# Performance work log

Measured on AMD Instinct MI355X. Metric: run time of the kernel, lower is better.

Reference implementation:

```python
import jax, jax.numpy as jnp
from jax import lax
import numpy as np

B, IN, J, S, F, O, C, KS = 8, 8, 8, 187, 64, 64, 67, 15


def _ln(x, eps=1e-5):
    m = jnp.mean(x, axis=-1, keepdims=True)
    v = jnp.mean((x - m) ** 2, axis=-1, keepdims=True)
    return (x - m) / jnp.sqrt(v + eps)


def setup_inputs() -> dict:
    key = jax.random.key(0)
    ks = jax.random.split(key, 8)
    x_in = jax.random.normal(ks[0], (B, IN, S, F), jnp.float32)
    proj_x_prev = jax.random.normal(ks[1], (B, IN, S, O), jnp.float32)
    lin = jnp.linspace(-1.0, 1.0, C, dtype=jnp.float32)
    spline_weights = jnp.broadcast_to(lin, (IN, J, C)) + 0.01 * jax.random.normal(ks[2], (IN, J, C), jnp.float32)
    tau = 0.1 * jax.random.normal(ks[3], (IN, J), jnp.float32) + 0.1
    temperature = jnp.asarray(1.0, jnp.float32)
    omiga = jnp.full((IN, J), 0.2, jnp.float32)
    W2 = jax.random.normal(ks[4], (J, F, O), jnp.float32) * (1.0 / np.sqrt(F))
    b_param = 0.02 * jax.random.normal(ks[5], (J, S, O), jnp.float32)
    ln_scale = jnp.ones((J, F), jnp.float32)
    ln_bias = jnp.zeros((J, F), jnp.float32)
    alpha = jnp.ones((J,), jnp.float32)
    beta = jnp.ones((J,), jnp.float32)
    theta = jnp.ones((J,), jnp.float32)
    gamma = jnp.ones((J,), jnp.float32)
    w3 = 0.1 * jax.random.normal(ks[6], (J, O, KS), jnp.float32)  # depthwise conv kernels
    return dict(x_in=x_in, proj_x_prev=proj_x_prev, spline_weights=spline_weights, tau=tau,
                temperature=temperature, omiga=omiga, W2=W2, b_param=b_param, ln_scale=ln_scale,
                ln_bias=ln_bias, alpha=alpha, beta=beta, theta=theta, gamma=gamma, w3=w3)


def reference(x_in, proj_x_prev, spline_weights, tau, temperature, omiga, W2, b_param,
              ln_scale, ln_bias, alpha, beta, theta, gamma, w3):
    b, in_n, seq, feat = x_in.shape
    out_n, nC = spline_weights.shape[1], spline_weights.shape[2]
    kk = w3.shape[-1]
    # --- cubic B-spline basis ---
    h = 2.0 / (nC - 1)
    grid = jnp.linspace(-1.0, 1.0, nC, dtype=x_in.dtype)
    max_val = jnp.max(jnp.abs(x_in)) + 1e-8
    xn = jnp.clip(x_in / max_val * 0.95, -0.99, 0.99)
    dist = jnp.abs(xn[..., None] - grid) / h  # [b,in,seq,feat,C]
    basis = jax.nn.relu(2.0 - dist) ** 3 / 6.0 - jax.nn.relu(1.0 - dist) ** 3 * (4.0 / 6.0)
    spline_mapping = jnp.einsum('bisfc,ijc->bijsf', basis, spline_weights)
    activated = spline_mapping + jnp.abs(omiga)[None, :, :, None, None] * x_in[:, :, None]
    # --- energy-threshold gating ---
    energies = jnp.mean(activated ** 2, axis=(-1, -2))  # [b,in,out]
    tau_a = jnp.abs(tau)[None]
    t_val = jnp.abs(temperature) * np.sqrt(seq / 256.0) + 1e-4
    sqrtE = jnp.sqrt(energies + 1e-8)
    mask = jax.nn.sigmoid((sqrtE - tau_a) / t_val)  # [b,in,out]
    mult = sqrtE / (tau_a + 1e-8)
    wp = proj_x_prev[:, :, None] * (mult * mask)[..., None, None]  # [b,in,out,seq,d]
    d = wp.shape[-1]
    mid = in_n // 2
    Kt = wp[:, 0::2].transpose(0, 2, 3, 1, 4).reshape(b, out_n, seq, mid * d)
    Qt = wp[:, 1::2].transpose(0, 2, 3, 1, 4).reshape(b, out_n, seq, mid * d)
    Kt, Qt = _ln(Kt), _ln(Qt)
    raw = jnp.einsum('bjse,bjte->bjst', Kt, Qt)
    W1 = jax.nn.softmax(raw / (np.sqrt(mid * d) * t_val), axis=-1)  # [b,out,seq,seq]
    combined = jnp.einsum('bijsf,bij->bjsf', activated, mask)  # [b,out,seq,feat]
    # --- SplineWeightLayer (vectorized over out_n) ---
    xln = _ln(combined) * ln_scale[None, :, None, :] + ln_bias[None, :, None, :]
    x_prime = jnp.einsum('bjsh,jho->bjso', xln, W2) + b_param[None]  # [b,out,seq,O]
    o = x_prime.shape[-1]
    xt = x_prime.transpose(0, 2, 1, 3).reshape(b, seq, out_n * o)
    ker = w3.transpose(2, 0, 1).reshape(kk, 1, out_n * o)
    w3f = lax.conv_general_dilated(xt, ker, (1,), [(kk // 2, kk // 2)],
                                   dimension_numbers=('NWC', 'WIO', 'NWC'),
                                   feature_group_count=out_n * o)
    w3f = w3f.reshape(b, seq, out_n, o).transpose(0, 2, 1, 3)
    eye = jnp.eye(seq, dtype=x_in.dtype)
    attn_kernel = jnp.abs(beta)[None, :, None, None] * W1 + jnp.abs(alpha)[None, :, None, None] * eye
    global_part = jnp.einsum('bjst,bjto->bjso', attn_kernel, x_prime)
    spatial = global_part + jnp.abs(theta)[None, :, None, None] * w3f
    out = spatial + gamma[None, :, None, None] * combined  # residual_proj is Identity (F==O)
    return out, x_prime
```

## Files before the change

kernel.cpp:

```cpp
#include <hip/hip_runtime.h>
#include <math.h>

#define B_N 8
#define IN_N 8
#define J_N 8
#define S_N 187
#define F_N 64
#define O_N 64
#define C_N 67
#define KS_N 15
#define SF_N (S_N * F_N)
#define E_N 256
#define ROWS_N (B_N * J_N * S_N)
#define SQRT_SF 0.85467470f

#define NT_SPL 47
#define NCOMB 376
#define NKTQT 2992
#define NRAW 576
#define NXPR 768
#define NMAXP 256

typedef __attribute__((ext_vector_type(8))) _Float16 half8;
typedef __attribute__((ext_vector_type(4))) _Float16 half4;
typedef __attribute__((ext_vector_type(4))) float floatx4;

__device__ __forceinline__ float wave_sum(float v) {
#pragma unroll
  for (int off = 32; off > 0; off >>= 1) v += __shfl_down(v, off, 64);
  return __shfl(v, 0, 64);
}
__device__ __forceinline__ float wave_max(float v) {
#pragma unroll
  for (int off = 32; off > 0; off >>= 1) v = fmaxf(v, __shfl_down(v, off, 64));
  return __shfl(v, 0, 64);
}
__device__ __forceinline__ float lane_bc(float v, int l) {
  return __int_as_float(__builtin_amdgcn_readlane(__float_as_int(v), l));
}
__device__ __forceinline__ float bspline(float d) {
  float t2 = fmaxf(2.f - d, 0.f);
  float t1 = fmaxf(1.f - d, 0.f);
  return t2 * t2 * t2 * (1.f / 6.f) - t1 * t1 * t1 * (4.f / 6.f);
}
__device__ __forceinline__ float get_inv095(const float* __restrict__ maxp) {
  int lane = threadIdx.x & 63;
  float m = 0.f;
#pragma unroll
  for (int k = 0; k < NMAXP / 64; k++) m = fmaxf(m, maxp[lane + k * 64]);
  return 0.95f / (wave_max(m) + 1e-8f);
}

__global__ void k_maxabs(const float4* __restrict__ x, float* __restrict__ maxp, int n4) {
  __shared__ float red[4];
  int tid = blockIdx.x * 256 + threadIdx.x;
  float m = 0.f;
  for (int i = tid; i < n4; i += gridDim.x * 256) {
    float4 v = x[i];
    m = fmaxf(m, fmaxf(fmaxf(fabsf(v.x), fabsf(v.y)), fmaxf(fabsf(v.z), fabsf(v.w))));
  }
  m = wave_max(m);
  if ((threadIdx.x & 63) == 0) red[threadIdx.x >> 6] = m;
  __syncthreads();
  if (threadIdx.x == 0)
    maxp[blockIdx.x] = fmaxf(fmaxf(red[0], red[1]), fmaxf(red[2], red[3]));
}

__global__ void k_spline(const float* __restrict__ x_in, const float* __restrict__ sw,
                         const float* __restrict__ omiga, const float* __restrict__ maxp,
                         float* __restrict__ act, float* __restrict__ esum_p) {
  int tile = blockIdx.x, bi = blockIdx.y;
  int i = bi & 7;
  __shared__ float wl[J_N * C_N];
  __shared__ float aom[J_N];
  __shared__ float red[4 * J_N];
  for (int t = threadIdx.x; t < J_N * C_N; t += 256) wl[t] = sw[i * J_N * C_N + t];
  if (threadIdx.x < J_N) aom[threadIdx.x] = fabsf(omiga[i * J_N + threadIdx.x]);
  int lane = threadIdx.x & 63, wid = threadIdx.x >> 6;
  float inv = get_inv095(maxp);
  __syncthreads();
  int idx = tile * 256 + threadIdx.x;
  float e[J_N] = {0, 0, 0, 0, 0, 0, 0, 0};
  if (idx < SF_N) {
    float x = x_in[(long)bi * SF_N + idx];
    float xn = fminf(fmaxf(x * inv, -0.99f), 0.99f);
    float u = (xn + 1.f) * 33.f;
    int c0 = (int)floorf(u) - 1;
    float sm[J_N] = {0, 0, 0, 0, 0, 0, 0, 0};
#pragma unroll
    for (int kk = 0; kk < 4; kk++) {
      int c = c0 + kk;
      if (c >= 0 && c < C_N) {
        float bas = bspline(fabsf(u - (float)c));
#pragma unroll
        for (int j = 0; j < J_N; j++) sm[j] += bas * wl[j * C_N + c];
      }
    }
#pragma unroll
    for (int j = 0; j < J_N; j++) {
      float a = sm[j] + aom[j] * x;
      act[((long)(bi * 8 + j)) * SF_N + idx] = a;
      e[j] = a * a;
    }
  }
#pragma unroll
  for (int j = 0; j < J_N; j++) {
    float v = e[j];
#pragma unroll
    for (int off = 32; off > 0; off >>= 1) v += __shfl_down(v, off, 64);
    if (lane == 0) red[wid * J_N + j] = v;
  }
  __syncthreads();
  if (threadIdx.x < J_N)
    esum_p[(long)(bi * 8 + threadIdx.x) * 48 + tile] =
        red[threadIdx.x] + red[8 + threadIdx.x] + red[16 + threadIdx.x] + red[24 + threadIdx.x];
}

__global__ void k_reduceE(const float* __restrict__ esum_p, const float* __restrict__ tau,
                          const float* __restrict__ temp, float* __restrict__ g_mask,
                          float* __restrict__ g_g) {
  int t = blockIdx.x * 256 + threadIdx.x;
  if (t >= 512) return;
  int i = (t >> 3) & 7, j = t & 7;
  const float* p = esum_p + (long)t * 48;
  float s = 0.f;
#pragma unroll
  for (int k = 0; k < NT_SPL; k++) s += p[k];
  float E = s * (1.f / (float)SF_N);
  float sE = sqrtf(E + 1e-8f);
  float ta = fabsf(tau[i * 8 + j]);
  float tv = fabsf(temp[0]) * SQRT_SF + 1e-4f;
  float mask = 1.f / (1.f + expf(-(sE - ta) / tv));
  g_mask[t] = mask;
  g_g[t] = (sE / (ta + 1e-8f)) * mask;
}

__global__ void k_mid2(const float* __restrict__ act, const float* __restrict__ g_mask,
                       const float* __restrict__ g_g, const float* __restrict__ proj,
                       float* __restrict__ comb,
                       _Float16* __restrict__ khi, _Float16* __restrict__ klo,
                       _Float16* __restrict__ qhi, _Float16* __restrict__ qlo) {
  __shared__ float mk[64];
  int lane = threadIdx.x & 63;
  if (blockIdx.x < NCOMB) {
    int b = blockIdx.x / 47, tile = blockIdx.x - b * 47;
    if (threadIdx.x < 64) mk[threadIdx.x] = g_mask[b * 64 + threadIdx.x];
    __syncthreads();
    int idx = tile * 256 + threadIdx.x;
    if (idx < SF_N) {
      float cb[J_N] = {0, 0, 0, 0, 0, 0, 0, 0};
#pragma unroll
      for (int i = 0; i < IN_N; i++) {
#pragma unroll
        for (int j = 0; j < J_N; j++)
          cb[j] += mk[i * 8 + j] * act[((long)((b * 8 + i) * 8 + j)) * SF_N + idx];
      }
#pragma unroll
      for (int j = 0; j < J_N; j++) comb[(b * J_N + j) * SF_N + idx] = cb[j];
    }
  } else {
    int w = threadIdx.x >> 6;
    int gr = (blockIdx.x - NCOMB) * 4 + w;
    int bj = gr / S_N, s = gr - bj * S_N;
    int b = bj >> 3, j = bj & 7;
    int ig = lane >> 4;
    int f4 = (lane & 15) * 4;
    int iK = b * 8 + 2 * ig;
    int iQ = iK + 1;
    float gK = g_g[iK * 8 + j];
    float gQ = g_g[iQ * 8 + j];
    float4 kr = *(const float4*)(proj + ((long)iK * S_N + s) * 64 + f4);
    float4 qr = *(const float4*)(proj + ((long)iQ * S_N + s) * 64 + f4);
    float kv[4] = {kr.x * gK, kr.y * gK, kr.z * gK, kr.w * gK};
    float qv[4] = {qr.x * gQ, qr.y * gQ, qr.z * gQ, qr.w * gQ};
    float mkv = wave_sum(kv[0] + kv[1] + kv[2] + kv[3]) * (1.f / 256.f);
    float mqv = wave_sum(qv[0] + qv[1] + qv[2] + qv[3]) * (1.f / 256.f);
    float vk = 0.f, vq = 0.f;
#pragma unroll
    for (int q = 0; q < 4; q++) {
      float dk = kv[q] - mkv; vk += dk * dk;
      float dq = qv[q] - mqv; vq += dq * dq;
    }
    vk = wave_sum(vk) * (1.f / 256.f);
    vq = wave_sum(vq) * (1.f / 256.f);
    float ik = 1.f / sqrtf(vk + 1e-5f);
    float iq = 1.f / sqrtf(vq + 1e-5f);
    long base = (long)gr * E_N + lane * 4;
    half4 hk4, lk4, hq4, lq4;
#pragma unroll
    for (int q = 0; q < 4; q++) {
      float fk = (kv[q] - mkv) * ik;
      float fq = (qv[q] - mqv) * iq;
      _Float16 hk = (_Float16)fk;
      _Float16 hq = (_Float16)fq;
      hk4[q] = hk; lk4[q] = (_Float16)(fk - (float)hk);
      hq4[q] = hq; lq4[q] = (_Float16)(fq - (float)hq);
    }
    *(half4*)(khi + base) = hk4;
    *(half4*)(klo + base) = lk4;
    *(half4*)(qhi + base) = hq4;
    *(half4*)(qlo + base) = lq4;
  }
}

__global__ void k_gemm(const _Float16* __restrict__ khi, const _Float16* __restrict__ klo,
                       const _Float16* __restrict__ qhi, const _Float16* __restrict__ qlo,
                       const float* __restrict__ temp, float* __restrict__ w1,
                       const float* __restrict__ comb, const float* __restrict__ W2,
                       const float* __restrict__ bparam, const float* __restrict__ lns,
                       const float* __restrict__ lnb, float* __restrict__ xprime) {
  __shared__ float smem[64 * 64 + 128];
  int lane = threadIdx.x & 63;
  if (blockIdx.x < NRAW) {
    int idx = blockIdx.x;
    int st = idx % 3, tt = (idx / 3) % 3, bj = idx / 9;
    int wave = threadIdx.x >> 6;
    int quad = lane >> 4, m16 = lane & 15;
    int ebase = quad * 8;
    int mrow = st * 64 + wave * 16 + m16;
    if (mrow > S_N - 1) mrow = S_N - 1;
    long aoff = ((long)bj * S_N + mrow) * E_N + ebase;
    const _Float16* ah_p = khi + aoff;
    const _Float16* al_p = klo + aoff;
    const _Float16* bh_p[4];
    const _Float16* bl_p[4];
#pragma unroll
    for (int n = 0; n < 4; n++) {
      int t = tt * 64 + n * 16 + m16;
      if (t > S_N - 1) t = S_N - 1;
      long boff = ((long)bj * S_N + t) * E_N + ebase;
      bh_p[n] = qhi + boff;
      bl_p[n] = qlo + boff;
    }
    floatx4 acc[4] = {};
    for (int ec = 0; ec < 8; ec++) {
      half8 ah = *(const half8*)(ah_p + ec * 32);
      half8 al = *(const half8*)(al_p + ec * 32);
#pragma unroll
      for (int n = 0; n < 4; n++) {
        half8 bh = *(const half8*)(bh_p[n] + ec * 32);
        half8 bl = *(const half8*)(bl_p[n] + ec * 32);
        acc[n] = __builtin_amdgcn_mfma_f32_16x16x32_f16(ah, bh, acc[n], 0, 0, 0);
        acc[n] = __builtin_amdgcn_mfma_f32_16x16x32_f16(al, bh, acc[n], 0, 0, 0);
        acc[n] = __builtin_amdgcn_mfma_f32_16x16x32_f16(ah, bl, acc[n], 0, 0, 0);
      }
    }
    float tv = fabsf(temp[0]) * SQRT_SF + 1e-4f;
    float scale = 1.f / (16.f * tv);
#pragma unroll
    for (int n = 0; n < 4; n++) {
      int t = tt * 64 + n * 16 + m16;
      if (t >= S_N) continue;
#pragma unroll
      for (int r = 0; r < 4; r++) {
        int s = st * 64 + wave * 16 + quad * 4 + r;
        if (s < S_N) w1[((long)bj * S_N + s) * S_N + t] = acc[n][r] * scale;
      }
    }
  } else {
    int q = blockIdx.x - NRAW;
    int tile = q % 12, bj = q / 12;
    int j = bj & 7;
    float* w2s = smem;
    float* lss = smem + 4096;
    float* lbs = smem + 4160;
    const float4* wg = (const float4*)(W2 + j * 4096);
    float4* ws4 = (float4*)w2s;
    for (int idx = threadIdx.x; idx < 1024; idx += 256) ws4[idx] = wg[idx];
    if (threadIdx.x < 64) {
      lss[threadIdx.x] = lns[j * 64 + threadIdx.x];
      lbs[threadIdx.x] = lnb[j * 64 + threadIdx.x];
    }
    __syncthreads();
    int w = threadIdx.x >> 6;
    int sbase = tile * 16 + w * 4;
    float xln[4], acc[4];
#pragma unroll
    for (int rr = 0; rr < 4; rr++) {
      int s = sbase + rr;
      int sc = (s < S_N) ? s : S_N - 1;
      float x = comb[((long)bj * S_N + sc) * 64 + lane];
      float m = wave_sum(x) * (1.f / 64.f);
      float d = x - m;
      float var = wave_sum(d * d) * (1.f / 64.f);
      xln[rr] = d / sqrtf(var + 1e-5f) * lss[lane] + lbs[lane];
      acc[rr] = bparam[(j * S_N + sc) * 64 + lane];
    }
#pragma unroll
    for (int h = 0; h < 64; h++) {
      float w2v = w2s[h * 64 + lane];
#pragma unroll
      for (int rr = 0; rr < 4; rr++) acc[rr] += lane_bc(xln[rr], h) * w2v;
    }
#pragma unroll
    for (int rr = 0; rr < 4; rr++) {
      int s = sbase + rr;
      if (s < S_N) xprime[((long)bj * S_N + s) * 64 + lane] = acc[rr];
    }
  }
}

__global__ void k_final(const float* __restrict__ xprime, const float* __restrict__ w1,
                        const float* __restrict__ comb, const float* __restrict__ w3,
                        const float* __restrict__ alpha, const float* __restrict__ beta,
                        const float* __restrict__ theta, const float* __restrict__ gamma,
                        float* __restrict__ out) {
  int tile = blockIdx.x, bj = blockIdx.y;
  int j = bj & 7;
  __shared__ float w1t[16 * 188];
  int s0 = tile * 16;
  for (int idx = threadIdx.x; idx < 16 * S_N; idx += 256) {
    int r = idx / S_N, t = idx - r * S_N;
    int srow = s0 + r;
    w1t[r * 188 + t] = (srow < S_N) ? w1[((long)bj * S_N + srow) * S_N + t] : 0.f;
  }
  __syncthreads();
  int w = threadIdx.x >> 6, o = threadIdx.x & 63;
#pragma unroll
  for (int rr = 0; rr < 4; rr++) {
    float* row = &w1t[(w * 4 + rr) * 188];
    float v[3];
    float m = -1e30f;
#pragma unroll
    for (int q = 0; q < 3; q++) {
      int t = o + q * 64;
      v[q] = (t < S_N) ? row[t] : -1e30f;
      m = fmaxf(m, v[q]);
    }
    m = wave_max(m);
    float ssum = 0.f;
#pragma unroll
    for (int q = 0; q < 3; q++) {
      int t = o + q * 64;
      float e = (t < S_N) ? expf(v[q] - m) : 0.f;
      v[q] = e;
      ssum += e;
    }
    ssum = wave_sum(ssum);
    float invs = 1.f / ssum;
#pragma unroll
    for (int q = 0; q < 3; q++) {
      int t = o + q * 64;
      if (t < S_N) row[t] = v[q] * invs;
    }
  }
  float w3c[KS_N];
#pragma unroll
  for (int k = 0; k < KS_N; k++) w3c[k] = w3[j * 64 * KS_N + o * KS_N + k];
  const float* xpg = xprime + (long)bj * (S_N * 64);
  float aa = fabsf(alpha[j]), ba = fabsf(beta[j]), ta = fabsf(theta[j]), gv = gamma[j];
  float acc[4] = {0.f, 0.f, 0.f, 0.f};
  for (int t = 0; t < 184; t += 4) {
    float x0 = xpg[t * 64 + o];
    float x1 = xpg[(t + 1) * 64 + o];
    float x2 = xpg[(t + 2) * 64 + o];
    float x3 = xpg[(t + 3) * 64 + o];
#pragma unroll
    for (int rr = 0; rr < 4; rr++) {
      float4 wv = *(const float4*)&w1t[(w * 4 + rr) * 188 + t];
      acc[rr] += wv.x * x0 + wv.y * x1 + wv.z * x2 + wv.w * x3;
    }
  }
#pragma unroll
  for (int t = 184; t < S_N; t++) {
    float xv = xpg[t * 64 + o];
#pragma unroll
    for (int rr = 0; rr < 4; rr++) acc[rr] += w1t[(w * 4 + rr) * 188 + t] * xv;
  }
#pragma unroll
  for (int rr = 0; rr < 4; rr++) {
    int s = s0 + w * 4 + rr;
    if (s >= S_N) continue;
    float conv = 0.f;
#pragma unroll
    for (int k = 0; k < KS_N; k++) {
      int si = s + k - 7;
      if (si >= 0 && si < S_N) conv += xpg[si * 64 + o] * w3c[k];
    }
    float res = ba * acc[rr] + aa * xpg[s * 64 + o] + ta * conv +
                gv * comb[((long)bj * S_N + s) * 64 + o];
    out[((long)bj * S_N + s) * 64 + o] = res;
  }
}

extern "C" void kernel_launch(void* const* d_in, const int* in_sizes, int n_in,
                              void* d_out, int out_size, void* d_ws, size_t ws_size,
                              hipStream_t stream) {
  const float* x_in   = (const float*)d_in[0];
  const float* proj   = (const float*)d_in[1];
  const float* sw     = (const float*)d_in[2];
  const float* tau    = (const float*)d_in[3];
  const float* temp   = (const float*)d_in[4];
  const float* omiga  = (const float*)d_in[5];
  const float* W2     = (const float*)d_in[6];
  const float* bparam = (const float*)d_in[7];
  const float* lns    = (const float*)d_in[8];
  const float* lnb    = (const float*)d_in[9];
  const float* alpha  = (const float*)d_in[10];
  const float* beta   = (const float*)d_in[11];
  const float* theta  = (const float*)d_in[12];
  const float* gamma  = (const float*)d_in[13];
  const float* w3     = (const float*)d_in[14];

  float* out = (float*)d_out;
  float* xprime = out + B_N * J_N * S_N * O_N;

  float* wsf = (float*)d_ws;
  float* maxp   = wsf;
  float* esum_p = wsf + 512;
  float* g_mask = wsf + 512 + 512 * 48;
  float* g_g    = g_mask + 512;
  float* act    = g_g + 512;
  const long RE = (long)ROWS_N * E_N;
  _Float16* khi = (_Float16*)(act + (long)64 * 8 * SF_N);
  _Float16* klo = khi + RE;
  _Float16* qhi = klo + RE;
  _Float16* qlo = qhi + RE;
  float* w1   = (float*)khi + 2 * RE;
  float* comb = w1 + (long)B_N * J_N * S_N * S_N;

  k_maxabs<<<NMAXP, 256, 0, stream>>>((const float4*)x_in, maxp, (B_N * IN_N * S_N * F_N) / 4);
  k_spline<<<dim3(NT_SPL, 64), 256, 0, stream>>>(x_in, sw, omiga, maxp, act, esum_p);
  k_reduceE<<<2, 256, 0, stream>>>(esum_p, tau, temp, g_mask, g_g);
  k_mid2<<<NCOMB + NKTQT, 256, 0, stream>>>(act, g_mask, g_g, proj, comb,
                                            khi, klo, qhi, qlo);
  k_gemm<<<NRAW + NXPR, 256, 0, stream>>>(khi, klo, qhi, qlo, temp, w1,
                                          comb, W2, bparam, lns, lnb, xprime);
  k_final<<<dim3(12, 64), 256, 0, stream>>>(xprime, w1, comb, w3, alpha, beta, theta, gamma, out);
}
```

Measured before the change: 176.7 us.

## Vectorize spline/combine, fold gate reduction into mid kernel, pre-swizzle MFMA fragments

The spline and combine stages now process four elements per thread with float4 loads and stores, using fewer blocks. The separate energy-reduction kernel is removed, and the mask and gate values are recomputed inside k_mid2 from the partial sums. The normalized K/Q fp16 hi/lo tensors are written straight into an MFMA fragment-ordered layout, with extra blocks zeroing the padded rows, so the GEMM reads contiguous half8 fragments without index clamping. This saves one launch and improves GEMM load coalescing, at the cost of redundant gate math in every row block and more buffer space.

```diff
diff --git a/kernel.cpp b/kernel.cpp
--- a/kernel.cpp
+++ b/kernel.cpp
@@ -10,16 +10,18 @@
 #define C_N 67
 #define KS_N 15
 #define SF_N (S_N * F_N)
+#define SF4_N (SF_N / 4)
 #define E_N 256
-#define ROWS_N (B_N * J_N * S_N)
 #define SQRT_SF 0.85467470f
 
-#define NT_SPL 47
-#define NCOMB 376
+#define NT_SPL 12
+#define NCOMB 96
 #define NKTQT 2992
+#define NZERO 16
 #define NRAW 576
 #define NXPR 768
 #define NMAXP 256
+#define FRAG_BJ 49152
 
 typedef __attribute__((ext_vector_type(8))) _Float16 half8;
 typedef __attribute__((ext_vector_type(4))) _Float16 half4;
@@ -49,6 +51,16 @@
 #pragma unroll
   for (int k = 0; k < NMAXP / 64; k++) m = fmaxf(m, maxp[lane + k * 64]);
   return 0.95f / (wave_max(m) + 1e-8f);
+}
+__device__ __forceinline__ float gate_g(const float* __restrict__ esum_p, int bi, int j,
+                                        const float* __restrict__ tau, float tv) {
+  const float* p = esum_p + ((long)bi * 8 + j) * NT_SPL;
+  float s = 0.f;
+#pragma unroll
+  for (int k = 0; k < NT_SPL; k++) s += p[k];
+  float sE = sqrtf(s * (1.f / (float)SF_N) + 1e-8f);
+  float ta = fabsf(tau[(bi & 7) * 8 + j]);
+  return (sE / (ta + 1e-8f)) / (1.f + expf(-(sE - ta) / tv));
 }
 
 __global__ void k_maxabs(const float4* __restrict__ x, float* __restrict__ maxp, int n4) {
@@ -66,9 +78,9 @@
     maxp[blockIdx.x] = fmaxf(fmaxf(red[0], red[1]), fmaxf(red[2], red[3]));
 }
 
-__global__ void k_spline(const float* __restrict__ x_in, const float* __restrict__ sw,
+__global__ void k_spline(const float4* __restrict__ x4, const float* __restrict__ sw,
                          const float* __restrict__ omiga, const float* __restrict__ maxp,
-                         float* __restrict__ act, float* __restrict__ esum_p) {
+                         float4* __restrict__ act4, float* __restrict__ esum_p) {
   int tile = blockIdx.x, bi = blockIdx.y;
   int i = bi & 7;
   __shared__ float wl[J_N * C_N];
@@ -79,29 +91,37 @@
   int lane = threadIdx.x & 63, wid = threadIdx.x >> 6;
   float inv = get_inv095(maxp);
   __syncthreads();
-  int idx = tile * 256 + threadIdx.x;
+  int i4 = tile * 256 + threadIdx.x;
   float e[J_N] = {0, 0, 0, 0, 0, 0, 0, 0};
-  if (idx < SF_N) {
-    float x = x_in[(long)bi * SF_N + idx];
-    float xn = fminf(fmaxf(x * inv, -0.99f), 0.99f);
-    float u = (xn + 1.f) * 33.f;
-    int c0 = (int)floorf(u) - 1;
-    float sm[J_N] = {0, 0, 0, 0, 0, 0, 0, 0};
-#pragma unroll
-    for (int kk = 0; kk < 4; kk++) {
-      int c = c0 + kk;
-      if (c >= 0 && c < C_N) {
-        float bas = bspline(fabsf(u - (float)c));
-#pragma unroll
-        for (int j = 0; j < J_N; j++) sm[j] += bas * wl[j * C_N + c];
+  if (i4 < SF4_N) {
+    float4 xv = x4[(long)bi * SF4_N + i4];
+    float xs[4] = {xv.x, xv.y, xv.z, xv.w};
+    float4 av[J_N];
+#pragma unroll
+    for (int c = 0; c < 4; c++) {
+      float x = xs[c];
+      float xn = fminf(fmaxf(x * inv, -0.99f), 0.99f);
+      float u = (xn + 1.f) * 33.f;
+      int c0 = (int)floorf(u) - 1;
+      float sm[J_N] = {0, 0, 0, 0, 0, 0, 0, 0};
+#pragma unroll
+      for (int kk = 0; kk < 4; kk++) {
+        int cc = c0 + kk;
+        if (cc >= 0 && cc < C_N) {
+          float bas = bspline(fabsf(u - (float)cc));
+#pragma unroll
+          for (int j = 0; j < J_N; j++) sm[j] += bas * wl[j * C_N + cc];
+        }
       }
-    }
-#pragma unroll
-    for (int j = 0; j < J_N; j++) {
-      float a = sm[j] + aom[j] * x;
-      act[((long)(bi * 8 + j)) * SF_N + idx] = a;
-      e[j] = a * a;
-    }
+#pragma unroll
+      for (int j = 0; j < J_N; j++) {
+        float a = sm[j] + aom[j] * x;
+        (&av[j].x)[c] = a;
+        e[j] += a * a;
+      }
+    }
+#pragma unroll
+    for (int j = 0; j < J_N; j++) act4[((long)(bi * 8 + j)) * SF4_N + i4] = av[j];
   }
 #pragma unroll
   for (int j = 0; j < J_N; j++) {
@@ -112,53 +132,48 @@
   }
   __syncthreads();
   if (threadIdx.x < J_N)
-    esum_p[(long)(bi * 8 + threadIdx.x) * 48 + tile] =
+    esum_p[((long)bi * 8 + threadIdx.x) * NT_SPL + tile] =
         red[threadIdx.x] + red[8 + threadIdx.x] + red[16 + threadIdx.x] + red[24 + threadIdx.x];
 }
 
-__global__ void k_reduceE(const float* __restrict__ esum_p, const float* __restrict__ tau,
-                          const float* __restrict__ temp, float* __restrict__ g_mask,
-                          float* __restrict__ g_g) {
-  int t = blockIdx.x * 256 + threadIdx.x;
-  if (t >= 512) return;
-  int i = (t >> 3) & 7, j = t & 7;
-  const float* p = esum_p + (long)t * 48;
-  float s = 0.f;
-#pragma unroll
-  for (int k = 0; k < NT_SPL; k++) s += p[k];
-  float E = s * (1.f / (float)SF_N);
-  float sE = sqrtf(E + 1e-8f);
-  float ta = fabsf(tau[i * 8 + j]);
-  float tv = fabsf(temp[0]) * SQRT_SF + 1e-4f;
-  float mask = 1.f / (1.f + expf(-(sE - ta) / tv));
-  g_mask[t] = mask;
-  g_g[t] = (sE / (ta + 1e-8f)) * mask;
-}
-
-__global__ void k_mid2(const float* __restrict__ act, const float* __restrict__ g_mask,
-                       const float* __restrict__ g_g, const float* __restrict__ proj,
-                       float* __restrict__ comb,
+__global__ void k_mid2(const float4* __restrict__ act4, const float* __restrict__ esum_p,
+                       const float* __restrict__ tau, const float* __restrict__ temp,
+                       const float* __restrict__ proj, float4* __restrict__ comb4,
                        _Float16* __restrict__ khi, _Float16* __restrict__ klo,
                        _Float16* __restrict__ qhi, _Float16* __restrict__ qlo) {
   __shared__ float mk[64];
   int lane = threadIdx.x & 63;
   if (blockIdx.x < NCOMB) {
-    int b = blockIdx.x / 47, tile = blockIdx.x - b * 47;
-    if (threadIdx.x < 64) mk[threadIdx.x] = g_mask[b * 64 + threadIdx.x];
+    int b = blockIdx.x / NT_SPL, tile = blockIdx.x - b * NT_SPL;
+    if (threadIdx.x < 64) {
+      int i = threadIdx.x >> 3, j = threadIdx.x & 7;
+      const float* p = esum_p + ((long)(b * 8 + i) * 8 + j) * NT_SPL;
+      float s = 0.f;
+#pragma unroll
+      for (int k = 0; k < NT_SPL; k++) s += p[k];
+      float sE = sqrtf(s * (1.f / (float)SF_N) + 1e-8f);
+      float ta = fabsf(tau[i * 8 + j]);
+      float tv = fabsf(temp[0]) * SQRT_SF + 1e-4f;
+      mk[threadIdx.x] = 1.f / (1.f + expf(-(sE - ta) / tv));
+    }
     __syncthreads();
-    int idx = tile * 256 + threadIdx.x;
-    if (idx < SF_N) {
-      float cb[J_N] = {0, 0, 0, 0, 0, 0, 0, 0};
+    int i4 = tile * 256 + threadIdx.x;
+    if (i4 < SF4_N) {
+      float4 cb[J_N] = {};
 #pragma unroll
       for (int i = 0; i < IN_N; i++) {
 #pragma unroll
-        for (int j = 0; j < J_N; j++)
-          cb[j] += mk[i * 8 + j] * act[((long)((b * 8 + i) * 8 + j)) * SF_N + idx];
+        for (int j = 0; j < J_N; j++) {
+          float4 a = act4[((long)((b * 8 + i) * 8 + j)) * SF4_N + i4];
+          float g = mk[i * 8 + j];
+          cb[j].x += g * a.x; cb[j].y += g * a.y;
+          cb[j].z += g * a.z; cb[j].w += g * a.w;
+        }
       }
 #pragma unroll
-      for (int j = 0; j < J_N; j++) comb[(b * J_N + j) * SF_N + idx] = cb[j];
-    }
-  } else {
+      for (int j = 0; j < J_N; j++) comb4[((long)(b * J_N + j)) * SF4_N + i4] = cb[j];
+    }
+  } else if (blockIdx.x < NCOMB + NKTQT) {
     int w = threadIdx.x >> 6;
     int gr = (blockIdx.x - NCOMB) * 4 + w;
     int bj = gr / S_N, s = gr - bj * S_N;
@@ -167,8 +182,9 @@
     int f4 = (lane & 15) * 4;
     int iK = b * 8 + 2 * ig;
     int iQ = iK + 1;
-    float gK = g_g[iK * 8 + j];
-    float gQ = g_g[iQ * 8 + j];
+    float tv = fabsf(temp[0]) * SQRT_SF + 1e-4f;
+    float gK = gate_g(esum_p, iK, j, tau, tv);
+    float gQ = gate_g(esum_p, iQ, j, tau, tv);
     float4 kr = *(const float4*)(proj + ((long)iK * S_N + s) * 64 + f4);
     float4 qr = *(const float4*)(proj + ((long)iQ * S_N + s) * 64 + f4);
     float kv[4] = {kr.x * gK, kr.y * gK, kr.z * gK, kr.w * gK};
@@ -185,7 +201,6 @@
     vq = wave_sum(vq) * (1.f / 256.f);
     float ik = 1.f / sqrtf(vk + 1e-5f);
     float iq = 1.f / sqrtf(vq + 1e-5f);
-    long base = (long)gr * E_N + lane * 4;
     half4 hk4, lk4, hq4, lq4;
 #pragma unroll
     for (int q = 0; q < 4; q++) {
@@ -196,10 +211,26 @@
       hk4[q] = hk; lk4[q] = (_Float16)(fk - (float)hk);
       hq4[q] = hq; lq4[q] = (_Float16)(fq - (float)hq);
     }
-    *(half4*)(khi + base) = hk4;
-    *(half4*)(klo + base) = lk4;
-    *(half4*)(qhi + base) = hq4;
-    *(half4*)(qlo + base) = lq4;
+    int stile = s >> 4, m16 = s & 15;
+    long fo = ((long)bj * 12 + stile) * 4096 + (lane >> 3) * 512 +
+              (((lane >> 1) & 3) * 16 + m16) * 8 + (lane & 1) * 4;
+    *(half4*)(khi + fo) = hk4;
+    *(half4*)(klo + fo) = lk4;
+    *(half4*)(qhi + fo) = hq4;
+    *(half4*)(qlo + fo) = lq4;
+  } else {
+    int zb = blockIdx.x - (NCOMB + NKTQT);
+    float4 z = {0.f, 0.f, 0.f, 0.f};
+    for (int t = zb * 256 + threadIdx.x; t < 10240; t += NZERO * 256) {
+      int bj = t / 160, r = t - bj * 160;
+      int ec = r / 20, rr = r - ec * 20;
+      int quad = rr / 5, m16 = 11 + rr - quad * 5;
+      long fo = ((long)bj * 12 + 11) * 4096 + ec * 512 + (quad * 16 + m16) * 8;
+      *(float4*)(khi + fo) = z;
+      *(float4*)(klo + fo) = z;
+      *(float4*)(qhi + fo) = z;
+      *(float4*)(qlo + fo) = z;
+    }
   }
 }
 
@@ -216,30 +247,19 @@
     int st = idx % 3, tt = (idx / 3) % 3, bj = idx / 9;
     int wave = threadIdx.x >> 6;
     int quad = lane >> 4, m16 = lane & 15;
-    int ebase = quad * 8;
-    int mrow = st * 64 + wave * 16 + m16;
-    if (mrow > S_N - 1) mrow = S_N - 1;
-    long aoff = ((long)bj * S_N + mrow) * E_N + ebase;
-    const _Float16* ah_p = khi + aoff;
-    const _Float16* al_p = klo + aoff;
-    const _Float16* bh_p[4];
-    const _Float16* bl_p[4];
-#pragma unroll
-    for (int n = 0; n < 4; n++) {
-      int t = tt * 64 + n * 16 + m16;
-      if (t > S_N - 1) t = S_N - 1;
-      long boff = ((long)bj * S_N + t) * E_N + ebase;
-      bh_p[n] = qhi + boff;
-      bl_p[n] = qlo + boff;
-    }
+    long fb = (long)bj * FRAG_BJ + lane * 8;
+    const _Float16* ah_p = khi + fb + (st * 4 + wave) * 4096;
+    const _Float16* al_p = klo + fb + (st * 4 + wave) * 4096;
+    const _Float16* bh_p = qhi + fb + tt * 4 * 4096;
+    const _Float16* bl_p = qlo + fb + tt * 4 * 4096;
     floatx4 acc[4] = {};
     for (int ec = 0; ec < 8; ec++) {
-      half8 ah = *(const half8*)(ah_p + ec * 32);
-      half8 al = *(const half8*)(al_p + ec * 32);
+      half8 ah = *(const half8*)(ah_p + ec * 512);
+      half8 al = *(const half8*)(al_p + ec * 512);
 #pragma unroll
       for (int n = 0; n < 4; n++) {
-        half8 bh = *(const half8*)(bh_p[n] + ec * 32);
-        half8 bl = *(const half8*)(bl_p[n] + ec * 32);
+        half8 bh = *(const half8*)(bh_p + n * 4096 + ec * 512);
+        half8 bl = *(const half8*)(bl_p + n * 4096 + ec * 512);
         acc[n] = __builtin_amdgcn_mfma_f32_16x16x32_f16(ah, bh, acc[n], 0, 0, 0);
         acc[n] = __builtin_amdgcn_mfma_f32_16x16x32_f16(al, bh, acc[n], 0, 0, 0);
         acc[n] = __builtin_amdgcn_mfma_f32_16x16x32_f16(ah, bl, acc[n], 0, 0, 0);
@@ -408,22 +428,20 @@
   float* wsf = (float*)d_ws;
   float* maxp   = wsf;
   float* esum_p = wsf + 512;
-  float* g_mask = wsf + 512 + 512 * 48;
-  float* g_g    = g_mask + 512;
-  float* act    = g_g + 512;
-  const long RE = (long)ROWS_N * E_N;
+  float* act    = wsf + 512 + 512 * NT_SPL;
+  const long FR = (long)64 * FRAG_BJ;
   _Float16* khi = (_Float16*)(act + (long)64 * 8 * SF_N);
-  _Float16* klo = khi + RE;
-  _Float16* qhi = klo + RE;
-  _Float16* qlo = qhi + RE;
-  float* w1   = (float*)khi + 2 * RE;
+  _Float16* klo = khi + FR;
+  _Float16* qhi = klo + FR;
+  _Float16* qlo = qhi + FR;
+  float* w1   = (float*)(qlo + FR);
   float* comb = w1 + (long)B_N * J_N * S_N * S_N;
 
   k_maxabs<<<NMAXP, 256, 0, stream>>>((const float4*)x_in, maxp, (B_N * IN_N * S_N * F_N) / 4);
-  k_spline<<<dim3(NT_SPL, 64), 256, 0, stream>>>(x_in, sw, omiga, maxp, act, esum_p);
-  k_reduceE<<<2, 256, 0, stream>>>(esum_p, tau, temp, g_mask, g_g);
-  k_mid2<<<NCOMB + NKTQT, 256, 0, stream>>>(act, g_mask, g_g, proj, comb,
-                                            khi, klo, qhi, qlo);
+  k_spline<<<dim3(NT_SPL, 64), 256, 0, stream>>>((const float4*)x_in, sw, omiga, maxp,
+                                                 (float4*)act, esum_p);
+  k_mid2<<<NCOMB + NKTQT + NZERO, 256, 0, stream>>>((const float4*)act, esum_p, tau, temp,
+                                                    proj, (float4*)comb, khi, klo, qhi, qlo);
   k_gemm<<<NRAW + NXPR, 256, 0, stream>>>(khi, klo, qhi, qlo, temp, w1,
                                           comb, W2, bparam, lns, lnb, xprime);
   k_final<<<dim3(12, 64), 256, 0, stream>>>(xprime, w1, comb, w3, alpha, beta, theta, gamma, out);
```

Measured after the change: 165.3 us. 6.4% less time.
